# Kernel tuning notes

Measured on AMD Instinct MI355X. Metric: run time of the kernel, lower is better.

Reference implementation:

```python
import jax, jax.numpy as jnp
import numpy as np

B, CIN, H, W = 4, 256, 56, 56
COUT, K = 256, 3
STRIDE, PAD, OG = 1, 1, 1
KK = K * K


def setup_inputs() -> dict:
    key = jax.random.key(0)
    k1, k2, k3, k4 = jax.random.split(key, 4)
    x = jax.random.normal(k1, (B, CIN, H, W), jnp.float32)
    # deformable conv weight [Cout, Cin/groups, K, K]
    weight = jax.random.normal(k2, (COUT, CIN, K, K), jnp.float32) * 0.05
    # offset-predicting 3x3 conv: 2*OG*K*K output channels (small init -> modest offsets)
    off_w = jax.random.normal(k3, (2 * OG * KK, CIN, 3, 3), jnp.float32) * 0.01
    off_b = jax.random.normal(k4, (2 * OG * KK,), jnp.float32) * 0.01
    return {"x": x, "weight": weight, "off_w": off_w, "off_b": off_b}


def _deform_conv(x, weight, off_w, off_b):
    Bn, C, Hh, Ww = x.shape
    # offset = param_generator(x): 3x3 conv, stride 1, pad 1
    offset = jax.lax.conv_general_dilated(
        x, off_w, window_strides=(1, 1), padding=((1, 1), (1, 1)),
        dimension_numbers=("NCHW", "OIHW", "NCHW")) + off_b[None, :, None, None]
    Ho = (Hh + 2 * PAD - K) // STRIDE + 1
    Wo = (Ww + 2 * PAD - K) // STRIDE + 1
    # torchvision layout: [B, OG, KK, (dy,dx), Ho, Wo]
    off = offset.reshape(Bn, OG, KK, 2, Ho, Wo)

    kh = jnp.arange(KK) // K
    kw = jnp.arange(KK) % K
    base_y = (jnp.arange(Ho) * STRIDE - PAD)[None, :, None] + kh[:, None, None]  # [KK,Ho,1]
    base_x = (jnp.arange(Wo) * STRIDE - PAD)[None, None, :] + kw[:, None, None]  # [KK,1,Wo]
    py = base_y[None, None].astype(x.dtype) + off[:, :, :, 0]  # [B,OG,KK,Ho,Wo]
    px = base_x[None, None].astype(x.dtype) + off[:, :, :, 1]

    Cg = C // OG
    xg = x.reshape(Bn, OG, Cg, Hh * Ww)

    def gather(yc, xc, wgt):
        # zero-padded bilinear corner: out-of-bounds samples contribute 0
        valid = (yc >= 0) & (yc < Hh) & (xc >= 0) & (xc < Ww)
        idx = (jnp.clip(yc, 0, Hh - 1) * Ww + jnp.clip(xc, 0, Ww - 1)).reshape(Bn, OG, 1, -1)
        v = jnp.take_along_axis(xg, idx, axis=3)            # [B,OG,Cg,KK*Ho*Wo]
        w = (wgt * valid.astype(wgt.dtype)).reshape(Bn, OG, 1, -1)
        return v * w

    y0 = jnp.floor(py).astype(jnp.int32)
    x0 = jnp.floor(px).astype(jnp.int32)
    ty = py - y0
    tx = px - x0
    sampled = (gather(y0,     x0,     (1 - ty) * (1 - tx))
             + gather(y0,     x0 + 1, (1 - ty) * tx)
             + gather(y0 + 1, x0,     ty * (1 - tx))
             + gather(y0 + 1, x0 + 1, ty * tx))
    sampled = sampled.reshape(Bn, C, KK, Ho, Wo)
    # weighted accumulation: implicit GEMM over (Cin, KK)
    return jnp.einsum("bikhw,oik->bohw", sampled, weight.reshape(COUT, C, KK))


def reference(x, weight, off_w, off_b):
    return _deform_conv(x, weight, off_w, off_b)
```

## Files before the change

### kernel.cpp

```cpp
#include <hip/hip_runtime.h>
#include <hip/hip_bf16.h>

#define B_N   4
#define CIN_  256
#define HH_   56
#define WW_   56
#define COUT_ 256
#define KK_   9
#define HW_   3136
#define KDIM  2304
#define NOFF  (B_N*18*HW_)
#define NOUT  (B_N*COUT_*HW_)

typedef __attribute__((ext_vector_type(8))) short short8;
typedef __attribute__((ext_vector_type(4))) float float4v;

__device__ __forceinline__ short f2bf_bits(float v) {
    union { __hip_bfloat16 h; short s; } u;
    u.h = __float2bfloat16(v);
    return u.s;
}
__device__ __forceinline__ float bfbits2f(short s) {
    union { unsigned u; float f; } u2;
    u2.u = ((unsigned)(unsigned short)s) << 16;
    return u2.f;
}

#define NB_AT  2304
#define NB_XT  784
#define NB_OW3 288
__global__ __launch_bounds__(256) void k_front(const float* __restrict__ x,
                                               const float* __restrict__ wgt,
                                               const float* __restrict__ ow,
                                               short* __restrict__ At,
                                               short* __restrict__ xTb,
                                               short* __restrict__ owT3) {
    __shared__ float tile[64][65];
    int bx = blockIdx.x;
    int t = threadIdx.x;
    if (bx < NB_AT) {
        int i = bx*256 + t;
        int o = i / KDIM; int r = i % KDIM;
        int kk = r >> 8;  int ci = r & 255;
        At[i] = f2bf_bits(wgt[(size_t)(o*CIN_ + ci)*9 + kk]);
        return;
    }
    if (bx < NB_AT + NB_XT) {
        int g = bx - NB_AT;
        int b = g / 196; int r = g % 196;
        int c0 = (r / 49) * 64; int p0 = (r % 49) * 64;
        int tp = t & 63;  int tc = t >> 6;
        #pragma unroll
        for (int i = 0; i < 16; ++i) {
            int ci = tc*16 + i;
            tile[ci][tp] = x[((size_t)b*CIN_ + c0 + ci)*HW_ + p0 + tp];
        }
        __syncthreads();
        #pragma unroll
        for (int i = 0; i < 16; ++i) {
            int p = tc*16 + i;
            xTb[((size_t)b*HW_ + p0 + p)*CIN_ + c0 + tp] = f2bf_bits(tile[tp][p]);
        }
        return;
    }
    {
        int i = (bx - NB_AT - NB_XT)*256 + t;
        int c = i / KDIM; int r = i % KDIM;
        int kk = r >> 8;  int ci = r & 255;
        owT3[i] = (c < 18) ? f2bf_bits(ow[(size_t)(c*CIN_ + ci)*9 + kk]) : 0;
    }
}

__global__ __launch_bounds__(256) void k_offgemm(const short* __restrict__ owT3,
                                                 const short* __restrict__ xTb,
                                                 float* __restrict__ pOff2) {
    __shared__ short sA[32*64];
    __shared__ short sB[64*64];
    __shared__ int   sP2[3*64];
    int t = threadIdx.x;
    int posb = blockIdx.x * 64;
    int b    = blockIdx.y;
    int ks   = blockIdx.z;
    int kt0  = ks * 768;
    int kend = kt0 + 768;

    for (int e = t; e < 3*64; e += 256) {
        int kk = ks*3 + (e >> 6); int row = e & 63;
        int pos = posb + row;
        int h = pos / WW_, w = pos % WW_;
        int yy = h + kk/3 - 1, xx = w + kk%3 - 1;
        bool v = (yy >= 0) && (yy < HH_) && (xx >= 0) && (xx < WW_);
        sP2[e] = v ? (yy*WW_ + xx) : -1;
    }
    __syncthreads();

    int arow = t >> 3,  aq  = t & 7;
    int brow = t >> 2,  bqc = (t & 3) * 2;

    int wv = t >> 6;
    int wm = (wv >> 1) * 16;
    int wn = (wv & 1) * 32;
    int lane = t & 63;
    int lm = lane & 15;
    int qd = lane >> 4;

    float4v acc[2];
    acc[0] = (float4v)(0.f); acc[1] = (float4v)(0.f);

    const short* gA = owT3 + (size_t)arow*KDIM + aq*8;
    const short* xb = xTb + (size_t)b*HW_*CIN_;

    short* wA = sA + (((arow >> 4)*8 + aq)*16 + ((arow + 2*aq) & 15))*8;
    short* wB[2];
    #pragma unroll
    for (int j = 0; j < 2; ++j) {
        int qq = bqc + j;
        wB[j] = sB + (((brow >> 4)*8 + qq)*16 + ((brow + 2*qq) & 15))*8;
    }

    short8 pa, pb[2];
    const short8 zero8 = (short8)(0);
    pa = *(const short8*)(gA + kt0);
    {
        int p2 = sP2[brow];
        #pragma unroll
        for (int j = 0; j < 2; ++j) {
            int ci0 = (kt0 & 255) + (bqc + j)*8;
            pb[j] = (p2 >= 0) ? *(const short8*)(xb + (size_t)p2*CIN_ + ci0) : zero8;
        }
    }

    for (int kt = kt0; kt < kend; kt += 64) {
        __syncthreads();
        *(short8*)wA = pa;
        #pragma unroll
        for (int j = 0; j < 2; ++j) *(short8*)wB[j] = pb[j];
        __syncthreads();
        int kt2 = kt + 64;
        if (kt2 < kend) {
            pa = *(const short8*)(gA + kt2);
            int kkl = (kt2 >> 8) - ks*3;
            int p2 = sP2[kkl*64 + brow];
            int cb = kt2 & 255;
            #pragma unroll
            for (int j = 0; j < 2; ++j) {
                int ci0 = cb + (bqc + j)*8;
                pb[j] = (p2 >= 0) ? *(const short8*)(xb + (size_t)p2*CIN_ + ci0) : zero8;
            }
        }
        #pragma unroll
        for (int kss = 0; kss < 2; ++kss) {
            int qe = kss*4 + qd;
            int sw = (lm + 2*qe) & 15;
            short8 af, bf[2];
            af = *(short8*)(sA + ((((wm>>4))*8 + qe)*16 + sw)*8);
            #pragma unroll
            for (int j = 0; j < 2; ++j)
                bf[j] = *(short8*)(sB + ((((wn>>4) + j)*8 + qe)*16 + sw)*8);
            #pragma unroll
            for (int j = 0; j < 2; ++j)
                acc[j] = __builtin_amdgcn_mfma_f32_16x16x32_bf16(
                             af, bf[j], acc[j], 0, 0, 0);
        }
    }

    float* pbase = pOff2 + (size_t)ks*NOFF;
    #pragma unroll
    for (int j = 0; j < 2; ++j) {
        int col = posb + wn + j*16 + lm;
        #pragma unroll
        for (int r = 0; r < 4; ++r) {
            int c = wm + qd*4 + r;
            if (c < 18)
                pbase[((size_t)(b*18 + c))*HW_ + col] = acc[j][r];
        }
    }
}

__global__ __launch_bounds__(256) void k_gemm(const short* __restrict__ At,
                                              const short* __restrict__ xTb,
                                              const float* __restrict__ pOff2,
                                              const float* __restrict__ ob,
                                              float* __restrict__ pout) {
    __shared__ short sA[128*64];
    __shared__ short sB[64*64];
    __shared__ int4   sPI[3*64];
    __shared__ float4 sPW[3*64];
    int t = threadIdx.x;

    int idx = blockIdx.x;
    int xcd = idx & 7;
    int b   = xcd & 3;
    int q   = (idx >> 3)*2 + (xcd >> 2);
    int m0   = (q & 1) * 128;
    int r2   = q >> 1;
    int posb = (r2 % 49) * 64;
    int ks   = r2 / 49;
    int kt0  = ks * 768;

    for (int e = t; e < 3*64; e += 256) {
        int kk = ks*3 + (e >> 6); int pl = e & 63;
        int pos = posb + pl;
        int h = pos / WW_, w = pos % WW_;
        size_t oy = (size_t)(b*18 + 2*kk    )*HW_ + pos;
        size_t ox = (size_t)(b*18 + 2*kk + 1)*HW_ + pos;
        float dy = ob[2*kk], dx = ob[2*kk + 1];
        #pragma unroll
        for (int s = 0; s < 3; ++s) {
            dy += pOff2[(size_t)s*NOFF + oy];
            dx += pOff2[(size_t)s*NOFF + ox];
        }
        float py = (float)(h - 1 + kk/3) + dy;
        float px = (float)(w - 1 + kk%3) + dx;
        float y0f = floorf(py), x0f = floorf(px);
        int y0 = (int)y0f, x0 = (int)x0f;
        float ty = py - y0f, tx = px - x0f;
        bool vy0 = (y0   >= 0) && (y0   < HH_);
        bool vy1 = (y0+1 >= 0) && (y0+1 < HH_);
        bool vx0 = (x0   >= 0) && (x0   < WW_);
        bool vx1 = (x0+1 >= 0) && (x0+1 < WW_);
        int y0c = min(max(y0,   0), HH_-1), y1c = min(max(y0+1, 0), HH_-1);
        int x0c = min(max(x0,   0), WW_-1), x1c = min(max(x0+1, 0), WW_-1);
        sPI[e] = make_int4(y0c*WW_+x0c, y0c*WW_+x1c, y1c*WW_+x0c, y1c*WW_+x1c);
        sPW[e] = make_float4((vy0 && vx0) ? (1.f-ty)*(1.f-tx) : 0.f,
                             (vy0 && vx1) ? (1.f-ty)*tx       : 0.f,
                             (vy1 && vx0) ? ty*(1.f-tx)       : 0.f,
                             (vy1 && vx1) ? ty*tx             : 0.f);
    }
    __syncthreads();

    int arow = t >> 1,  aqc = (t & 1) * 4;
    int brow = t >> 2,  bqc = (t & 3) * 2;

    int wv = t >> 6;
    int wm = (wv >> 1) * 64;
    int wn = (wv & 1) * 32;
    int lane = t & 63;
    int lm = lane & 15;
    int qd = lane >> 4;

    float4v acc[4][2];
    #pragma unroll
    for (int i = 0; i < 4; ++i)
        #pragma unroll
        for (int j = 0; j < 2; ++j) acc[i][j] = (float4v)(0.f);

    const short* gA = At + (size_t)(m0 + arow)*KDIM + aqc*8;
    const short* xb = xTb + (size_t)b*HW_*CIN_;

    short* wA[4]; short* wB[2];
    #pragma unroll
    for (int j = 0; j < 4; ++j) {
        int qq = aqc + j;
        wA[j] = sA + (((arow >> 4)*8 + qq)*16 + ((arow + 2*qq) & 15))*8;
    }
    #pragma unroll
    for (int j = 0; j < 2; ++j) {
        int qq = bqc + j;
        wB[j] = sB + (((brow >> 4)*8 + qq)*16 + ((brow + 2*qq) & 15))*8;
    }

    short8 pa[4];
    short8 cgA[2][4], cgB[2][4];
    float4 bwA, bwB;

#define PALOAD(itX) do {                                                      \
    _Pragma("unroll")                                                         \
    for (int j = 0; j < 4; ++j)                                               \
        pa[j] = *(const short8*)(gA + kt0 + (itX)*64 + j*8);                  \
} while (0)

#define CGLOAD(cg, bw, itX) do {                                              \
    int4 id_ = sPI[((itX) >> 2)*64 + brow];                                   \
    bw = sPW[((itX) >> 2)*64 + brow];                                         \
    int cb_ = ((itX) & 3) * 64;                                               \
    _Pragma("unroll")                                                         \
    for (int j = 0; j < 2; ++j) {                                             \
        int ci0_ = cb_ + (bqc + j)*8;                                         \
        cg[j][0] = *(const short8*)(xb + (size_t)id_.x*CIN_ + ci0_);          \
        cg[j][1] = *(const short8*)(xb + (size_t)id_.y*CIN_ + ci0_);          \
        cg[j][2] = *(const short8*)(xb + (size_t)id_.z*CIN_ + ci0_);          \
        cg[j][3] = *(const short8*)(xb + (size_t)id_.w*CIN_ + ci0_);          \
    }                                                                         \
} while (0)

#define GSTEP(cg, bw, it) do {                                                \
    short8 pk[2];                                                             \
    _Pragma("unroll")                                                         \
    for (int j = 0; j < 2; ++j) {                                             \
        float f[8];                                                           \
        _Pragma("unroll")                                                     \
        for (int e = 0; e < 8; ++e)                                           \
            f[e] = bw.x*bfbits2f(cg[j][0][e]) + bw.y*bfbits2f(cg[j][1][e])    \
                 + bw.z*bfbits2f(cg[j][2][e]) + bw.w*bfbits2f(cg[j][3][e]);   \
        union { short8 s8; __hip_bfloat162 h2[4]; } pu;                       \
        _Pragma("unroll")                                                     \
        for (int e2 = 0; e2 < 4; ++e2)                                        \
            pu.h2[e2] = __float22bfloat162_rn(make_float2(f[2*e2], f[2*e2+1]));\
        pk[j] = pu.s8;                                                        \
    }                                                                         \
    __syncthreads();                            \
    _Pragma("unroll")                                                         \
    for (int j = 0; j < 4; ++j) *(short8*)wA[j] = pa[j];                      \
    _Pragma("unroll")                                                         \
    for (int j = 0; j < 2; ++j) *(short8*)wB[j] = pk[j];                      \
    __syncthreads();                                                          \
    if ((it) + 1 < 12) PALOAD((it) + 1);                                      \
    if ((it) + 2 < 12) CGLOAD(cg, bw, (it) + 2);                              \
    _Pragma("unroll")                                                         \
    for (int kss = 0; kss < 2; ++kss) {                                       \
        int qe = kss*4 + qd;                                                  \
        int sw = (lm + 2*qe) & 15;                                            \
        short8 af[4], bf[2];                                                  \
        _Pragma("unroll")                                                     \
        for (int i = 0; i < 4; ++i)                                           \
            af[i] = *(short8*)(sA + ((((wm>>4) + i)*8 + qe)*16 + sw)*8);      \
        _Pragma("unroll")                                                     \
        for (int j = 0; j < 2; ++j)                                           \
            bf[j] = *(short8*)(sB + ((((wn>>4) + j)*8 + qe)*16 + sw)*8);      \
        _Pragma("unroll")                                                     \
        for (int i = 0; i < 4; ++i)                                           \
            _Pragma("unroll")                                                 \
            for (int j = 0; j < 2; ++j)                                       \
                acc[i][j] = __builtin_amdgcn_mfma_f32_16x16x32_bf16(          \
                                af[i], bf[j], acc[i][j], 0, 0, 0);            \
    }                                                                         \
} while (0)

    PALOAD(0);
    CGLOAD(cgA, bwA, 0);
    CGLOAD(cgB, bwB, 1);

    for (int it2 = 0; it2 < 6; ++it2) {
        GSTEP(cgA, bwA, it2*2);
        GSTEP(cgB, bwB, it2*2 + 1);
    }

#undef PALOAD
#undef CGLOAD
#undef GSTEP

    float* pbase = pout + (size_t)ks*NOUT;
    #pragma unroll
    for (int i = 0; i < 4; ++i)
        #pragma unroll
        for (int j = 0; j < 2; ++j) {
            int col = posb + wn + j*16 + lm;
            #pragma unroll
            for (int r = 0; r < 4; ++r) {
                int m = m0 + wm + i*16 + qd*4 + r;
                pbase[((size_t)b*COUT_ + m)*HW_ + col] = acc[i][j][r];
            }
        }
}

__global__ __launch_bounds__(256) void k_oreduce(const float* __restrict__ pout,
                                                 float* __restrict__ out) {
    int i = blockIdx.x*256 + threadIdx.x;
    if (i >= NOUT/4) return;
    float4 a = ((const float4*)pout)[i];
    float4 b = ((const float4*)(pout + NOUT))[i];
    float4 c = ((const float4*)(pout + 2*(size_t)NOUT))[i];
    float4 r;
    r.x = a.x + b.x + c.x;  r.y = a.y + b.y + c.y;
    r.z = a.z + b.z + c.z;  r.w = a.w + b.w + c.w;
    ((float4*)out)[i] = r;
}

extern "C" void kernel_launch(void* const* d_in, const int* in_sizes, int n_in,
                              void* d_out, int out_size, void* d_ws, size_t ws_size,
                              hipStream_t stream) {
    const float* x   = (const float*)d_in[0];
    const float* wgt = (const float*)d_in[1];
    const float* ow  = (const float*)d_in[2];
    const float* ob  = (const float*)d_in[3];
    float* out = (float*)d_out;

    char* ws = (char*)d_ws;
    short* At    = (short*)ws;
    short* xTb   = (short*)(ws + 1179648);
    short* owT3  = (short*)(ws + 7602176);
    float* pOff2 = (float*)(ws + 7749632);
    float* pout  = (float*)(ws + 10459136);

    k_front  <<<dim3(NB_AT + NB_XT + NB_OW3), 256, 0, stream>>>(x, wgt, ow, At, xTb, owT3);
    k_offgemm<<<dim3(49, 4, 3),               256, 0, stream>>>(owT3, xTb, pOff2);
    k_gemm   <<<dim3(1176),                   256, 0, stream>>>(At, xTb, pOff2, ob, pout);
    k_oreduce<<<dim3(NOUT/4/256),             256, 0, stream>>>(pout, out);
}
```

Measured before the change: 137.9 us.

## Pre-swizzle weights into MFMA fragment layout and double-buffer LDS in both GEMMs

The weight matrix is now written by the front kernel directly in per-lane MFMA fragment order, so the main GEMM loads A fragments straight from global memory into registers and no longer stages A through LDS. Both the offset GEMM and the main GEMM switch to double-buffered LDS for B, which halves the barriers per k-step and lets the next tile's global loads overlap compute. The cost is more live registers (eight A fragments per step) and uncached-by-LDS global reads of A that every wave repeats, which may raise L2 traffic.

```diff
diff --git a/kernel.cpp b/kernel.cpp
--- a/kernel.cpp
+++ b/kernel.cpp
@@ -32,7 +32,7 @@
 __global__ __launch_bounds__(256) void k_front(const float* __restrict__ x,
                                                const float* __restrict__ wgt,
                                                const float* __restrict__ ow,
-                                               short* __restrict__ At,
+                                               short* __restrict__ At2,
                                                short* __restrict__ xTb,
                                                short* __restrict__ owT3) {
     __shared__ float tile[64][65];
@@ -40,9 +40,15 @@
     int t = threadIdx.x;
     if (bx < NB_AT) {
         int i = bx*256 + t;
-        int o = i / KDIM; int r = i % KDIM;
-        int kk = r >> 8;  int ci = r & 255;
-        At[i] = f2bf_bits(wgt[(size_t)(o*CIN_ + ci)*9 + kk]);
+        int e = i & 7;
+        int l = (i >> 3) & 63;
+        int gg = i >> 9;
+        int g  = gg % 72;
+        int rt = gg / 72;
+        int m = rt*16 + (l & 15);
+        int k = g*32 + (l >> 4)*8 + e;
+        int kk = k >> 8;  int ci = k & 255;
+        At2[i] = f2bf_bits(wgt[(size_t)(m*CIN_ + ci)*9 + kk]);
         return;
     }
     if (bx < NB_AT + NB_XT) {
@@ -74,15 +80,14 @@
 __global__ __launch_bounds__(256) void k_offgemm(const short* __restrict__ owT3,
                                                  const short* __restrict__ xTb,
                                                  float* __restrict__ pOff2) {
-    __shared__ short sA[32*64];
-    __shared__ short sB[64*64];
+    __shared__ short sA[2*32*64];
+    __shared__ short sB[2*64*64];
     __shared__ int   sP2[3*64];
     int t = threadIdx.x;
     int posb = blockIdx.x * 64;
     int b    = blockIdx.y;
     int ks   = blockIdx.z;
     int kt0  = ks * 768;
-    int kend = kt0 + 768;
 
     for (int e = t; e < 3*64; e += 256) {
         int kk = ks*3 + (e >> 6); int row = e & 63;
@@ -110,59 +115,60 @@
     const short* gA = owT3 + (size_t)arow*KDIM + aq*8;
     const short* xb = xTb + (size_t)b*HW_*CIN_;
 
-    short* wA = sA + (((arow >> 4)*8 + aq)*16 + ((arow + 2*aq) & 15))*8;
-    short* wB[2];
+    int wAo = (((arow >> 4)*8 + aq)*16 + ((arow + 2*aq) & 15))*8;
+    int wBo[2];
     #pragma unroll
     for (int j = 0; j < 2; ++j) {
         int qq = bqc + j;
-        wB[j] = sB + (((brow >> 4)*8 + qq)*16 + ((brow + 2*qq) & 15))*8;
-    }
-
-    short8 pa, pb[2];
+        wBo[j] = (((brow >> 4)*8 + qq)*16 + ((brow + 2*qq) & 15))*8;
+    }
+
     const short8 zero8 = (short8)(0);
-    pa = *(const short8*)(gA + kt0);
-    {
-        int p2 = sP2[brow];
-        #pragma unroll
-        for (int j = 0; j < 2; ++j) {
-            int ci0 = (kt0 & 255) + (bqc + j)*8;
-            pb[j] = (p2 >= 0) ? *(const short8*)(xb + (size_t)p2*CIN_ + ci0) : zero8;
-        }
-    }
-
-    for (int kt = kt0; kt < kend; kt += 64) {
-        __syncthreads();
-        *(short8*)wA = pa;
-        #pragma unroll
-        for (int j = 0; j < 2; ++j) *(short8*)wB[j] = pb[j];
-        __syncthreads();
-        int kt2 = kt + 64;
-        if (kt2 < kend) {
-            pa = *(const short8*)(gA + kt2);
-            int kkl = (kt2 >> 8) - ks*3;
-            int p2 = sP2[kkl*64 + brow];
-            int cb = kt2 & 255;
-            #pragma unroll
-            for (int j = 0; j < 2; ++j) {
-                int ci0 = cb + (bqc + j)*8;
-                pb[j] = (p2 >= 0) ? *(const short8*)(xb + (size_t)p2*CIN_ + ci0) : zero8;
-            }
-        }
-        #pragma unroll
-        for (int kss = 0; kss < 2; ++kss) {
-            int qe = kss*4 + qd;
-            int sw = (lm + 2*qe) & 15;
-            short8 af, bf[2];
-            af = *(short8*)(sA + ((((wm>>4))*8 + qe)*16 + sw)*8);
-            #pragma unroll
-            for (int j = 0; j < 2; ++j)
-                bf[j] = *(short8*)(sB + ((((wn>>4) + j)*8 + qe)*16 + sw)*8);
-            #pragma unroll
-            for (int j = 0; j < 2; ++j)
-                acc[j] = __builtin_amdgcn_mfma_f32_16x16x32_bf16(
-                             af, bf[j], acc[j], 0, 0, 0);
-        }
-    }
+    short8 paA, paB, pbA[2], pbB[2];
+
+#define PLOAD(pa, pb, itX) do {                                               \
+    pa = *(const short8*)(gA + kt0 + (itX)*64);                               \
+    int p2_ = sP2[((itX) >> 2)*64 + brow];                                    \
+    int cb_ = ((itX) & 3) * 64;                                               \
+    _Pragma("unroll")                                                         \
+    for (int j = 0; j < 2; ++j) {                                             \
+        int ci0_ = cb_ + (bqc + j)*8;                                         \
+        pb[j] = (p2_ >= 0) ? *(const short8*)(xb + (size_t)p2_*CIN_ + ci0_)   \
+                           : zero8;                                           \
+    }                                                                         \
+} while (0)
+
+#define OSTEP(pa, pb, it, bs) do {                                            \
+    *(short8*)(sA + (bs)*2048 + wAo) = pa;                                    \
+    _Pragma("unroll")                                                         \
+    for (int j = 0; j < 2; ++j) *(short8*)(sB + (bs)*4096 + wBo[j]) = pb[j];  \
+    if ((it) + 2 < 12) PLOAD(pa, pb, (it) + 2);                               \
+    __syncthreads();                                                          \
+    _Pragma("unroll")                                                         \
+    for (int kss = 0; kss < 2; ++kss) {                                       \
+        int qe = kss*4 + qd;                                                  \
+        int sw = (lm + 2*qe) & 15;                                            \
+        short8 af, bf[2];                                                     \
+        af = *(short8*)(sA + (bs)*2048 + ((((wm>>4))*8 + qe)*16 + sw)*8);     \
+        _Pragma("unroll")                                                     \
+        for (int j = 0; j < 2; ++j)                                           \
+            bf[j] = *(short8*)(sB + (bs)*4096 +                               \
+                               ((((wn>>4) + j)*8 + qe)*16 + sw)*8);           \
+        _Pragma("unroll")                                                     \
+        for (int j = 0; j < 2; ++j)                                           \
+            acc[j] = __builtin_amdgcn_mfma_f32_16x16x32_bf16(                 \
+                         af, bf[j], acc[j], 0, 0, 0);                         \
+    }                                                                         \
+} while (0)
+
+    PLOAD(paA, pbA, 0);
+    PLOAD(paB, pbB, 1);
+    for (int it2 = 0; it2 < 6; ++it2) {
+        OSTEP(paA, pbA, it2*2,     0);
+        OSTEP(paB, pbB, it2*2 + 1, 1);
+    }
+#undef PLOAD
+#undef OSTEP
 
     float* pbase = pOff2 + (size_t)ks*NOFF;
     #pragma unroll
@@ -177,13 +183,12 @@
     }
 }
 
-__global__ __launch_bounds__(256) void k_gemm(const short* __restrict__ At,
+__global__ __launch_bounds__(256) void k_gemm(const short* __restrict__ At2,
                                               const short* __restrict__ xTb,
                                               const float* __restrict__ pOff2,
                                               const float* __restrict__ ob,
                                               float* __restrict__ pout) {
-    __shared__ short sA[128*64];
-    __shared__ short sB[64*64];
+    __shared__ short sB[2*64*64];
     __shared__ int4   sPI[3*64];
     __shared__ float4 sPW[3*64];
     int t = threadIdx.x;
@@ -196,7 +201,6 @@
     int r2   = q >> 1;
     int posb = (r2 % 49) * 64;
     int ks   = r2 / 49;
-    int kt0  = ks * 768;
 
     for (int e = t; e < 3*64; e += 256) {
         int kk = ks*3 + (e >> 6); int pl = e & 63;
@@ -229,7 +233,6 @@
     }
     __syncthreads();
 
-    int arow = t >> 1,  aqc = (t & 1) * 4;
     int brow = t >> 2,  bqc = (t & 3) * 2;
 
     int wv = t >> 6;
@@ -245,30 +248,19 @@
         #pragma unroll
         for (int j = 0; j < 2; ++j) acc[i][j] = (float4v)(0.f);
 
-    const short* gA = At + (size_t)(m0 + arow)*KDIM + aqc*8;
     const short* xb = xTb + (size_t)b*HW_*CIN_;
-
-    short* wA[4]; short* wB[2];
-    #pragma unroll
-    for (int j = 0; j < 4; ++j) {
-        int qq = aqc + j;
-        wA[j] = sA + (((arow >> 4)*8 + qq)*16 + ((arow + 2*qq) & 15))*8;
-    }
+    const short* pA = At2 + (((size_t)((m0 + wm) >> 4) * 72) << 9) + (size_t)lane * 8;
+    int g0 = ks * 24;
+
+    int wBo[2];
     #pragma unroll
     for (int j = 0; j < 2; ++j) {
         int qq = bqc + j;
-        wB[j] = sB + (((brow >> 4)*8 + qq)*16 + ((brow + 2*qq) & 15))*8;
-    }
-
-    short8 pa[4];
+        wBo[j] = (((brow >> 4)*8 + qq)*16 + ((brow + 2*qq) & 15))*8;
+    }
+
     short8 cgA[2][4], cgB[2][4];
     float4 bwA, bwB;
-
-#define PALOAD(itX) do {                                                      \
-    _Pragma("unroll")                                                         \
-    for (int j = 0; j < 4; ++j)                                               \
-        pa[j] = *(const short8*)(gA + kt0 + (itX)*64 + j*8);                  \
-} while (0)
 
 #define CGLOAD(cg, bw, itX) do {                                              \
     int4 id_ = sPI[((itX) >> 2)*64 + brow];                                   \
@@ -284,7 +276,14 @@
     }                                                                         \
 } while (0)
 
-#define GSTEP(cg, bw, it) do {                                                \
+#define GSTEP(cg, bw, it, bs) do {                                            \
+    short8 af[8];                                                             \
+    _Pragma("unroll")                                                         \
+    for (int kss = 0; kss < 2; ++kss)                                         \
+        _Pragma("unroll")                                                     \
+        for (int i = 0; i < 4; ++i)                                           \
+            af[kss*4 + i] = *(const short8*)(                                 \
+                pA + ((size_t)(i*72 + g0 + (it)*2 + kss) << 9));              \
     short8 pk[2];                                                             \
     _Pragma("unroll")                                                         \
     for (int j = 0; j < 2; ++j) {                                             \
@@ -299,44 +298,34 @@
             pu.h2[e2] = __float22bfloat162_rn(make_float2(f[2*e2], f[2*e2+1]));\
         pk[j] = pu.s8;                                                        \
     }                                                                         \
-    __syncthreads();                            \
-    _Pragma("unroll")                                                         \
-    for (int j = 0; j < 4; ++j) *(short8*)wA[j] = pa[j];                      \
-    _Pragma("unroll")                                                         \
-    for (int j = 0; j < 2; ++j) *(short8*)wB[j] = pk[j];                      \
+    if ((it) + 2 < 12) CGLOAD(cg, bw, (it) + 2);     \
+    _Pragma("unroll")                                                         \
+    for (int j = 0; j < 2; ++j) *(short8*)(sB + (bs)*4096 + wBo[j]) = pk[j];  \
     __syncthreads();                                                          \
-    if ((it) + 1 < 12) PALOAD((it) + 1);                                      \
-    if ((it) + 2 < 12) CGLOAD(cg, bw, (it) + 2);                              \
     _Pragma("unroll")                                                         \
     for (int kss = 0; kss < 2; ++kss) {                                       \
         int qe = kss*4 + qd;                                                  \
         int sw = (lm + 2*qe) & 15;                                            \
-        short8 af[4], bf[2];                                                  \
-        _Pragma("unroll")                                                     \
-        for (int i = 0; i < 4; ++i)                                           \
-            af[i] = *(short8*)(sA + ((((wm>>4) + i)*8 + qe)*16 + sw)*8);      \
+        short8 bf[2];                                                         \
         _Pragma("unroll")                                                     \
         for (int j = 0; j < 2; ++j)                                           \
-            bf[j] = *(short8*)(sB + ((((wn>>4) + j)*8 + qe)*16 + sw)*8);      \
+            bf[j] = *(short8*)(sB + (bs)*4096 +                               \
+                               ((((wn>>4) + j)*8 + qe)*16 + sw)*8);           \
         _Pragma("unroll")                                                     \
         for (int i = 0; i < 4; ++i)                                           \
             _Pragma("unroll")                                                 \
             for (int j = 0; j < 2; ++j)                                       \
                 acc[i][j] = __builtin_amdgcn_mfma_f32_16x16x32_bf16(          \
-                                af[i], bf[j], acc[i][j], 0, 0, 0);            \
+                                af[kss*4 + i], bf[j], acc[i][j], 0, 0, 0);    \
     }                                                                         \
 } while (0)
 
-    PALOAD(0);
     CGLOAD(cgA, bwA, 0);
     CGLOAD(cgB, bwB, 1);
-
     for (int it2 = 0; it2 < 6; ++it2) {
-        GSTEP(cgA, bwA, it2*2);
-        GSTEP(cgB, bwB, it2*2 + 1);
-    }
-
-#undef PALOAD
+        GSTEP(cgA, bwA, it2*2,     0);
+        GSTEP(cgB, bwB, it2*2 + 1, 1);
+    }
 #undef CGLOAD
 #undef GSTEP
 
@@ -377,14 +366,14 @@
     float* out = (float*)d_out;
 
     char* ws = (char*)d_ws;
-    short* At    = (short*)ws;
+    short* At2   = (short*)ws;
     short* xTb   = (short*)(ws + 1179648);
     short* owT3  = (short*)(ws + 7602176);
     float* pOff2 = (float*)(ws + 7749632);
     float* pout  = (float*)(ws + 10459136);
 
-    k_front  <<<dim3(NB_AT + NB_XT + NB_OW3), 256, 0, stream>>>(x, wgt, ow, At, xTb, owT3);
+    k_front  <<<dim3(NB_AT + NB_XT + NB_OW3), 256, 0, stream>>>(x, wgt, ow, At2, xTb, owT3);
     k_offgemm<<<dim3(49, 4, 3),               256, 0, stream>>>(owT3, xTb, pOff2);
-    k_gemm   <<<dim3(1176),                   256, 0, stream>>>(At, xTb, pOff2, ob, pout);
+    k_gemm   <<<dim3(1176),                   256, 0, stream>>>(At2, xTb, pOff2, ob, pout);
     k_oreduce<<<dim3(NOUT/4/256),             256, 0, stream>>>(pout, out);
 }
```

Result: faster. 131.8 us (-4.5%).
